# Kernel tuning notes

Hardware: AMD Instinct MI355X
Metric: run time of the kernel (lower is better)

The kernel has to match this reference:

```python
import jax, jax.numpy as jnp
import numpy as np

N = 20000        # number of protein atoms
C_IN = 32        # input atom features
C = 128          # hidden_channels
E_BOND = 80000   # directed bond edges (~2 bonds/atom, both directions)
R = 4.0          # radius_graph radius (Angstrom)
BOX = 55.0       # box side -> ~32 neighbors within r=4


def _radius_graph_np(pos, r):
    # symmetric radius graph, no self loops (PyG radius_graph, neighbor cap omitted)
    r2 = r * r
    rows, cols = [], []
    for i0 in range(0, pos.shape[0], 500):
        chunk = pos[i0:i0 + 500]
        d2 = ((chunk[:, None, :] - pos[None, :, :]) ** 2).sum(-1)
        m = d2 < r2
        m[np.arange(chunk.shape[0]), i0 + np.arange(chunk.shape[0])] = False
        ii, jj = np.nonzero(m)
        rows.append(jj)            # source j
        cols.append(ii + i0)       # target i
    return np.stack([np.concatenate(rows), np.concatenate(cols)]).astype(np.int32)


def setup_inputs() -> dict:
    key = jax.random.key(0)
    ks = jax.random.split(key, 12)
    rng = np.random.default_rng(0)

    pos = rng.uniform(0.0, BOX, (N, 3)).astype(np.float32)
    r_edge_index = jnp.asarray(_radius_graph_np(pos, R))

    half = E_BOND // 2
    s = rng.integers(0, N, half); d = rng.integers(0, N, half)
    edge_index = jnp.asarray(np.stack([np.concatenate([s, d]), np.concatenate([d, s])]).astype(np.int32))

    def lin(k, fin, fout):
        lim = 1.0 / np.sqrt(fin)
        kw, kb = jax.random.split(k)
        W = jax.random.uniform(kw, (fin, fout), jnp.float32, -lim, lim)
        b = jax.random.uniform(kb, (fout,), jnp.float32, -lim, lim)
        return W, b

    We1, be1 = lin(ks[0], C_IN, C)
    We2, be2 = lin(ks[1], C, C)
    Wf1, bf1 = lin(ks[2], 2 * C, C); Ws1, bs1 = lin(ks[3], 2 * C, C)
    Wf2, bf2 = lin(ks[4], 2 * C, C); Ws2, bs2 = lin(ks[5], 2 * C, C)
    Wf3, bf3 = lin(ks[6], 2 * C, C); Ws3, bs3 = lin(ks[7], 2 * C, C)
    Wf4, bf4 = lin(ks[8], 2 * C, C); Ws4, bs4 = lin(ks[9], 2 * C, C)

    x_prot = jax.random.normal(ks[10], (N, C_IN), jnp.float32)
    v_prot = jnp.asarray(pos)

    return dict(x_prot=x_prot, v_prot=v_prot, edge_index=edge_index, r_edge_index=r_edge_index,
                We1=We1, be1=be1, We2=We2, be2=be2,
                Wf1=Wf1, bf1=bf1, Ws1=Ws1, bs1=bs1,
                Wf2=Wf2, bf2=bf2, Ws2=Ws2, bs2=bs2,
                Wf3=Wf3, bf3=bf3, Ws3=Ws3, bs3=bs3,
                Wf4=Wf4, bf4=bf4, Ws4=Ws4, bs4=bs4)


def _cgconv(x, ei, Wf, bf, Ws, bs):
    # PyG CGConv: z = [x_i, x_j]; out = x + mean_j sigmoid(lin_f(z)) * softplus(lin_s(z))
    src, dst = ei[0], ei[1]              # source j -> target i
    z = jnp.concatenate([x[dst], x[src]], axis=1)          # [E, 2C]
    msg = jax.nn.sigmoid(z @ Wf + bf) * jax.nn.softplus(z @ Ws + bs)  # [E, C]
    agg = jax.ops.segment_sum(msg, dst, num_segments=x.shape[0])
    cnt = jax.ops.segment_sum(jnp.ones((ei.shape[1],), x.dtype), dst, num_segments=x.shape[0])
    return x + agg / jnp.maximum(cnt, 1.0)[:, None]


def reference(x_prot, v_prot, edge_index, r_edge_index,
              We1, be1, We2, be2,
              Wf1, bf1, Ws1, bs1, Wf2, bf2, Ws2, bs2,
              Wf3, bf3, Ws3, bs3, Wf4, bf4, Ws4, bs4):
    # embed MLP (PyG MLP with batch-norm at init == identity): Linear->ReLU->Linear
    x = jax.nn.relu(x_prot @ We1 + be1) @ We2 + be2
    # bond convs
    x = jax.nn.relu(_cgconv(x, edge_index, Wf1, bf1, Ws1, bs1))
    x = jax.nn.relu(_cgconv(x, edge_index, Wf2, bf2, Ws2, bs2))
    # radius convs (r_edge_index = radius_graph(v_prot, r=4), precomputed in setup)
    x = jax.nn.relu(_cgconv(x, r_edge_index, Wf3, bf3, Ws3, bs3))
    x = jax.nn.relu(_cgconv(x, r_edge_index, Wf4, bf4, Ws4, bs4))
    return jax.nn.relu(x)  # final self.act (idempotent on ReLU output)
```

## Files before the change

### kernel.cpp

```cpp
#include <hip/hip_runtime.h>
#include <hip/hip_bf16.h>

#define NN 20000
#define CC 128

typedef __attribute__((ext_vector_type(8))) _Float16 half8;
typedef __attribute__((ext_vector_type(2))) _Float16 half2v;
typedef __attribute__((ext_vector_type(4))) float f32x4;

typedef const __attribute__((address_space(1))) void gv_t;
typedef __attribute__((address_space(3))) void sv_t;

__global__ __launch_bounds__(256) void conv_all_kernel(
    const float* __restrict__ Wf0, const float* __restrict__ Ws0,
    const float* __restrict__ Wf1, const float* __restrict__ Ws1,
    const float* __restrict__ Wf2, const float* __restrict__ Ws2,
    const float* __restrict__ Wf3, const float* __restrict__ Ws3,
    const float* __restrict__ We2, const float* __restrict__ We1,
    const float* __restrict__ xprot,
    _Float16* __restrict__ WctAll, _Float16* __restrict__ Wcte,
    _Float16* __restrict__ Wt1, _Float16* __restrict__ xp16) {
    int id = blockIdx.x * 256 + threadIdx.x;
    if (id < 262144) {
        int Lw = id >> 16;
        int i = id & 65535;
        int c = i & 511;
        int k = i >> 9;
        const float* Wfp = (Lw == 0) ? Wf0 : (Lw == 1) ? Wf1 : (Lw == 2) ? Wf2 : Wf3;
        const float* Wsp = (Lw == 0) ? Ws0 : (Lw == 1) ? Ws1 : (Lw == 2) ? Ws2 : Ws3;
        float v;
        if (c < 128) v = Wfp[k * 128 + c];
        else if (c < 256) v = Wfp[(128 + k) * 128 + (c - 128)];
        else if (c < 384) v = Wsp[k * 128 + (c - 256)];
        else v = Wsp[(128 + k) * 128 + (c - 384)];
        WctAll[Lw * 65536 + c * 128 + k] = (_Float16)v;
    } else if (id < 278528) {
        int i = id - 262144;
        int c = i & 127;
        int k = i >> 7;
        Wcte[c * 128 + k] = (_Float16)We2[k * 128 + c];
    } else if (id < 282624) {
        int i = id - 278528;
        int c = i & 127;
        int k = i >> 7;
        Wt1[c * 32 + k] = (_Float16)We1[k * 128 + c];
    } else {
        int i = id - 282624;
        xp16[i] = (_Float16)xprot[i];
    }
}

__global__ __launch_bounds__(256) void enc1_mfma_kernel(
    const _Float16* __restrict__ A, const _Float16* __restrict__ Wt1,
    const float* __restrict__ b, _Float16* __restrict__ Y) {
    int t = threadIdx.x;
    int wid = t >> 6, l = t & 63;
    int lr = l & 15, hi = l >> 4;
    int m0 = blockIdx.x * 128 + wid * 32;
    half8 af[2];
#pragma unroll
    for (int m = 0; m < 2; ++m) {
        int row = m0 + m * 16 + lr;
        half8 v = {0, 0, 0, 0, 0, 0, 0, 0};
        if (row < NN) v = *(const half8*)(A + (long)row * 32 + hi * 8);
        af[m] = v;
    }
    f32x4 acc[2][8] = {};
#pragma unroll
    for (int n = 0; n < 8; ++n) {
        int col = n * 16 + lr;
        half8 bg = *(const half8*)(Wt1 + (long)col * 32 + hi * 8);
#pragma unroll
        for (int m = 0; m < 2; ++m)
            acc[m][n] = __builtin_amdgcn_mfma_f32_16x16x32_f16(af[m], bg, acc[m][n], 0, 0, 0);
    }
#pragma unroll
    for (int n = 0; n < 8; ++n) {
        int col = n * 16 + lr;
        float bb = b[col];
#pragma unroll
        for (int m = 0; m < 2; ++m) {
#pragma unroll
            for (int q = 0; q < 4; ++q) {
                int row = m0 + m * 16 + hi * 4 + q;
                if (row < NN)
                    Y[(long)row * 128 + col] = (_Float16)fmaxf(acc[m][n][q] + bb, 0.0f);
            }
        }
    }
}

__global__ __launch_bounds__(256) void gemm_mfma_kernel(
    const _Float16* __restrict__ A, const _Float16* __restrict__ Wt,
    const float* __restrict__ bias0, const float* __restrict__ bias1,
    char* __restrict__ outH, float* __restrict__ outF,
    _Float16* __restrict__ outF16, int M, int mode) {
    __shared__ _Float16 lds[32768];
    int t = threadIdx.x;
    int w = t >> 6, l = t & 63;
    int m0 = blockIdx.x * 128;
    int n0 = blockIdx.y * 128;
    {
        int rin = l >> 4;
        int cs = l & 15;
#pragma unroll
        for (int j = 0; j < 8; ++j) {
            int r = w * 32 + j * 4 + rin;
            int g = cs ^ (r & 7);
            int grow = m0 + r;
            if (grow > M - 1) grow = M - 1;
            __builtin_amdgcn_global_load_lds((gv_t*)(A + (long)grow * 128 + g * 8),
                (sv_t*)&lds[(w * 32 + j * 4) * 128], 16, 0, 0);
            __builtin_amdgcn_global_load_lds((gv_t*)(Wt + (long)(n0 + r) * 128 + g * 8),
                (sv_t*)&lds[16384 + (w * 32 + j * 4) * 128], 16, 0, 0);
        }
    }
    __syncthreads();
    int wm = w >> 1, wn = w & 1;
    int lr = l & 15, hi = l >> 4;
    f32x4 acc[4][4] = {};
#pragma unroll
    for (int ks = 0; ks < 4; ++ks) {
        int cidx = 4 * ks + hi;
        half8 af[4], bg[4];
#pragma unroll
        for (int m = 0; m < 4; ++m) {
            int row = wm * 64 + m * 16 + lr;
            af[m] = *(const half8*)(&lds[row * 128 + (cidx ^ (row & 7)) * 8]);
        }
#pragma unroll
        for (int n = 0; n < 4; ++n) {
            int row = wn * 64 + n * 16 + lr;
            bg[n] = *(const half8*)(&lds[16384 + row * 128 + (cidx ^ (row & 7)) * 8]);
        }
#pragma unroll
        for (int m = 0; m < 4; ++m)
#pragma unroll
            for (int n = 0; n < 4; ++n)
                acc[m][n] = __builtin_amdgcn_mfma_f32_16x16x32_f16(
                    af[m], bg[n], acc[m][n], 0, 0, 0);
    }
    if (mode == 0) {
        __syncthreads();
        const float S = 1.44269504f;
        bool isSrc = (n0 == 128) || (n0 == 384);
        float sgn = (n0 == 128) ? -S : S;
#pragma unroll
        for (int n = 0; n < 4; ++n) {
            int cl = wn * 64 + n * 16 + lr;
            int gcol = n0 + cl;
            float badd = (gcol < 128) ? bias0[gcol]
                       : ((gcol >= 256 && gcol < 384) ? bias1[gcol - 256] : 0.0f);
#pragma unroll
            for (int m = 0; m < 4; ++m)
#pragma unroll
                for (int q = 0; q < 4; ++q) {
                    int rl = wm * 64 + m * 16 + hi * 4 + q;
                    float v = acc[m][n][q] + badd;
                    if (!isSrc) {
                        lds[rl * 144 + cl] = (_Float16)(v * S);
                    } else {
                        float p = __builtin_amdgcn_exp2f(v * sgn);
                        uint b = __float_as_uint(p);
                        b = (b + 0x7FFFu + ((b >> 16) & 1u)) >> 16;
                        ((ushort*)lds)[rl * 144 + cl] = (ushort)b;
                    }
                }
        }
        __syncthreads();
        int base = (n0 == 0) ? 0 : (n0 == 128) ? 512 : (n0 == 256) ? 256 : 768;
#pragma unroll
        for (int i = 0; i < 8; ++i) {
            int id = t + 256 * i;
            int row = id >> 4, ch = id & 15;
            int grow = m0 + row;
            if (grow < M) {
                half8 v = *(const half8*)(&lds[row * 144 + ch * 8]);
                *(half8*)(outH + (long)grow * 1024 + base + ch * 16) = v;
            }
        }
    } else {
#pragma unroll
        for (int n = 0; n < 4; ++n) {
            int gcol = n0 + wn * 64 + n * 16 + lr;
            float badd = bias0[gcol];
#pragma unroll
            for (int m = 0; m < 4; ++m)
#pragma unroll
                for (int q = 0; q < 4; ++q) {
                    int grow = m0 + wm * 64 + m * 16 + hi * 4 + q;
                    if (grow < M) {
                        float v = acc[m][n][q] + badd;
                        outF[(long)grow * 128 + gcol] = v;
                        outF16[(long)grow * 128 + gcol] = (_Float16)v;
                    }
                }
        }
    }
}

__global__ __launch_bounds__(256) void count_int_kernel(
    const int* __restrict__ dst, int E, int* __restrict__ cnt) {
    int e = blockIdx.x * 256 + threadIdx.x;
    if (e < E) atomicAdd(&cnt[dst[e]], 1);
}

__global__ __launch_bounds__(1024) void scan_kernel(
    const int* __restrict__ cnt, int* __restrict__ off) {
    __shared__ int part[1024];
    int t = threadIdx.x;
    int base = t * 20;
    int loc[20];
    int s = 0;
#pragma unroll
    for (int i = 0; i < 20; ++i) {
        int idx = base + i;
        int v = (idx < NN) ? cnt[idx] : 0;
        loc[i] = s;
        s += v;
    }
    part[t] = s;
    __syncthreads();
    for (int d = 1; d < 1024; d <<= 1) {
        int v = (t >= d) ? part[t - d] : 0;
        __syncthreads();
        part[t] += v;
        __syncthreads();
    }
    int pre = (t > 0) ? part[t - 1] : 0;
#pragma unroll
    for (int i = 0; i < 20; ++i) {
        int idx = base + i;
        if (idx < NN) off[idx] = pre + loc[i];
    }
    if (t == 1023) off[NN] = part[1023];
}

__global__ __launch_bounds__(256) void scatter_kernel(
    const int* __restrict__ src, const int* __restrict__ dst, int E,
    const int* __restrict__ off, int* __restrict__ cur, int* __restrict__ eid) {
    int e = blockIdx.x * 256 + threadIdx.x;
    if (e < E) {
        int d = dst[e];
        int p = off[d] + atomicAdd(&cur[d], 1);
        eid[p] = src[e];
    }
}

__global__ __launch_bounds__(256) void csr_off_kernel(
    const int* __restrict__ dst, int E, int N1, int* __restrict__ off) {
    int n = blockIdx.x * 256 + threadIdx.x;
    if (n >= N1) return;
    int lo = 0, hi = E;
    while (lo < hi) {
        int mid = (lo + hi) >> 1;
        if (dst[mid] < n) lo = mid + 1;
        else hi = mid;
    }
    off[n] = lo;
}

__global__ __launch_bounds__(256) void node_agg_kernel(
    const char* __restrict__ H, const int* __restrict__ srcArr,
    const int* __restrict__ off, const float* __restrict__ xin,
    float* __restrict__ xout, _Float16* __restrict__ xh, int write_h) {
    int n = blockIdx.x * 4 + (threadIdx.x >> 6);
    int nu = __builtin_amdgcn_readfirstlane(n);
    int l = threadIdx.x & 63;
    const char* hb = H + (long)nu * 1024;
    half2v fdh = *(const half2v*)(hb + l * 4);
    half2v sdh = *(const half2v*)(hb + 256 + l * 4);
    float vd0 = __builtin_amdgcn_exp2f(-(float)fdh.x);
    float vd1 = __builtin_amdgcn_exp2f(-(float)fdh.y);
    float ud0 = __builtin_amdgcn_exp2f((float)sdh.x);
    float ud1 = __builtin_amdgcn_exp2f((float)sdh.y);
    int e0 = __builtin_amdgcn_readfirstlane(off[nu]);
    int e1 = __builtin_amdgcn_readfirstlane(off[nu + 1]);
    float ax = 0.0f, ay = 0.0f;
#define EDGEC(w0, w1)                                                        \
    {                                                                        \
        float vs0 = __uint_as_float((w0) << 16);                             \
        float vs1 = __uint_as_float((w0) & 0xFFFF0000u);                     \
        float us0 = __uint_as_float((w1) << 16);                             \
        float us1 = __uint_as_float((w1) & 0xFFFF0000u);                     \
        float rx = __builtin_amdgcn_rcpf(__builtin_fmaf(vd0, vs0, 1.0f));    \
        float ry = __builtin_amdgcn_rcpf(__builtin_fmaf(vd1, vs1, 1.0f));    \
        float px = __builtin_amdgcn_logf(__builtin_fmaf(ud0, us0, 1.0f));    \
        float py = __builtin_amdgcn_logf(__builtin_fmaf(ud1, us1, 1.0f));    \
        ax = __builtin_fmaf(rx, px, ax);                                     \
        ay = __builtin_fmaf(ry, py, ay);                                     \
    }
    int e = e0;
    for (; e + 7 < e1; e += 8) {
        uint wv[8], wu[8];
#pragma unroll
        for (int j = 0; j < 8; ++j) {
            int s = srcArr[e + j];
            const char* hs = H + (long)s * 1024 + (long)l * 4;
            wv[j] = *(const uint*)(hs + 512);
            wu[j] = *(const uint*)(hs + 768);
        }
#pragma unroll
        for (int j = 0; j < 8; ++j) EDGEC(wv[j], wu[j])
    }
    for (; e < e1; ++e) {
        int s = srcArr[e];
        const char* hs = H + (long)s * 1024 + (long)l * 4;
        uint w0 = *(const uint*)(hs + 512);
        uint w1 = *(const uint*)(hs + 768);
        EDGEC(w0, w1)
    }
#undef EDGEC
    float inv = 0.6931471805599453f *
                __builtin_amdgcn_rcpf(fmaxf((float)(e1 - e0), 1.0f));
    float2 xv = ((const float2*)xin)[(long)nu * 64 + l];
    float ox = fmaxf(xv.x + ax * inv, 0.0f);
    float oy = fmaxf(xv.y + ay * inv, 0.0f);
    ((float2*)xout)[(long)nu * 64 + l] = make_float2(ox, oy);
    if (write_h) {
        half2v oh;
        oh.x = (_Float16)ox;
        oh.y = (_Float16)oy;
        ((half2v*)xh)[(long)nu * 64 + l] = oh;
    }
}

extern "C" void kernel_launch(void* const* d_in, const int* in_sizes, int n_in,
                              void* d_out, int out_size, void* d_ws, size_t ws_size,
                              hipStream_t stream) {
    const float* x_prot = (const float*)d_in[0];
    const int* eb = (const int*)d_in[2];
    const int* er = (const int*)d_in[3];
    int Eb = in_sizes[2] / 2;
    int Er = in_sizes[3] / 2;
    const float* We1 = (const float*)d_in[4];
    const float* be1 = (const float*)d_in[5];
    const float* We2 = (const float*)d_in[6];
    const float* be2 = (const float*)d_in[7];
    const float* Wf[4]  = {(const float*)d_in[8],  (const float*)d_in[12],
                           (const float*)d_in[16], (const float*)d_in[20]};
    const float* bf[4]  = {(const float*)d_in[9],  (const float*)d_in[13],
                           (const float*)d_in[17], (const float*)d_in[21]};
    const float* Wsp[4] = {(const float*)d_in[10], (const float*)d_in[14],
                           (const float*)d_in[18], (const float*)d_in[22]};
    const float* bsp[4] = {(const float*)d_in[11], (const float*)d_in[15],
                           (const float*)d_in[19], (const float*)d_in[23]};

    char* ws = (char*)d_ws;
    float*     xbuf  = (float*)ws;
    _Float16*  xhf   = (_Float16*)(ws + 10240000);
    char*      H     = (char*)(ws + 15360000);
    _Float16*  xp16  = (_Float16*)(ws + 35840000);
    int*       cntI  = (int*)(ws + 37120000);
    int*       curB  = (int*)(ws + 37200000);
    int*       offB  = (int*)(ws + 37280000);
    int*       offR  = (int*)(ws + 37360016);
    int*       eidB  = (int*)(ws + 37440032);
    _Float16*  WctAll= (_Float16*)(ws + 37760032);
    _Float16*  Wcte  = (_Float16*)(ws + 38284320);
    _Float16*  Wt1   = (_Float16*)(ws + 38317088);

    const int* srcB = eb;
    const int* dstB = eb + Eb;
    const int* srcR = er;

    conv_all_kernel<<<3604, 256, 0, stream>>>(
        Wf[0], Wsp[0], Wf[1], Wsp[1], Wf[2], Wsp[2], Wf[3], Wsp[3],
        We2, We1, x_prot, WctAll, Wcte, Wt1, xp16);

    hipMemsetAsync(cntI, 0, 160000, stream);
    count_int_kernel<<<(Eb + 255) / 256, 256, 0, stream>>>(dstB, Eb, cntI);
    scan_kernel<<<1, 1024, 0, stream>>>(cntI, offB);
    scatter_kernel<<<(Eb + 255) / 256, 256, 0, stream>>>(srcB, dstB, Eb, offB, curB, eidB);
    csr_off_kernel<<<(NN + 256) / 256, 256, 0, stream>>>(er + Er, Er, NN + 1, offR);

    enc1_mfma_kernel<<<157, 256, 0, stream>>>(xp16, Wt1, be1, (_Float16*)H);
    {
        dim3 g(157, 1);
        gemm_mfma_kernel<<<g, 256, 0, stream>>>((_Float16*)H, Wcte, be2, be2,
                                                nullptr, xbuf, xhf, NN, 1);
    }

    for (int L = 0; L < 4; ++L) {
        dim3 g(157, 4);
        gemm_mfma_kernel<<<g, 256, 0, stream>>>(xhf, WctAll + L * 65536, bf[L],
                                                bsp[L], H, nullptr, nullptr, NN, 0);
        const int* sArr = (L < 2) ? eidB : srcR;
        const int* oArr = (L < 2) ? offB : offR;
        float* xout = (L == 3) ? (float*)d_out : xbuf;
        node_agg_kernel<<<NN / 4, 256, 0, stream>>>(H, sArr, oArr, xbuf, xout,
                                                    xhf, (L == 3) ? 0 : 1);
    }
    (void)n_in; (void)out_size; (void)ws_size;
}
```

Before: 243.1 us.

## Interleave source H halves, drop fp32 residual buffer, double-buffer edge gathers

The GEMM epilogue now interleaves the two source-side halves of H so each lane fetches one 8-byte word per neighbor instead of two 4-byte loads. The fp32 residual copy of x is removed, and node aggregation reads and updates the fp16 x in place, writing fp32 only for the final layer. The edge loop is restructured to prefetch the next batch of 8 neighbors while computing the current one, with a 4-wide remainder path. Together these cut gather transactions and residual traffic but add fp16 rounding of the residual stream between layers. The in-place update relies on the GEMM having consumed x before aggregation runs.

Measured after the change: 269.8 us. 1.11x slower.

```diff
diff --git a/kernel.cpp b/kernel.cpp
--- a/kernel.cpp
+++ b/kernel.cpp
@@ -93,8 +93,7 @@
 __global__ __launch_bounds__(256) void gemm_mfma_kernel(
     const _Float16* __restrict__ A, const _Float16* __restrict__ Wt,
     const float* __restrict__ bias0, const float* __restrict__ bias1,
-    char* __restrict__ outH, float* __restrict__ outF,
-    _Float16* __restrict__ outF16, int M, int mode) {
+    char* __restrict__ outH, _Float16* __restrict__ outF16, int M, int mode) {
     __shared__ _Float16 lds[32768];
     int t = threadIdx.x;
     int w = t >> 6, l = t & 63;
@@ -168,15 +167,23 @@
                 }
         }
         __syncthreads();
-        int base = (n0 == 0) ? 0 : (n0 == 128) ? 512 : (n0 == 256) ? 256 : 768;
+        bool isSrc2 = (n0 == 128) || (n0 == 384);
 #pragma unroll
         for (int i = 0; i < 8; ++i) {
             int id = t + 256 * i;
             int row = id >> 4, ch = id & 15;
             int grow = m0 + row;
-            if (grow < M) {
-                half8 v = *(const half8*)(&lds[row * 144 + ch * 8]);
-                *(half8*)(outH + (long)grow * 1024 + base + ch * 16) = v;
+            if (grow >= M) continue;
+            half8 v = *(const half8*)(&lds[row * 144 + ch * 8]);
+            if (!isSrc2) {
+                int b2 = (n0 == 0) ? 0 : 256;
+                *(half8*)(outH + (long)grow * 1024 + b2 + ch * 16) = v;
+            } else {
+                const uint* vp = (const uint*)&v;
+                char* bp = outH + (long)grow * 1024 + 512 + ch * 32 +
+                           ((n0 == 384) ? 4 : 0);
+#pragma unroll
+                for (int j = 0; j < 4; ++j) *(uint*)(bp + j * 8) = vp[j];
             }
         }
     } else {
@@ -189,11 +196,9 @@
 #pragma unroll
                 for (int q = 0; q < 4; ++q) {
                     int grow = m0 + wm * 64 + m * 16 + hi * 4 + q;
-                    if (grow < M) {
-                        float v = acc[m][n][q] + badd;
-                        outF[(long)grow * 128 + gcol] = v;
-                        outF16[(long)grow * 128 + gcol] = (_Float16)v;
-                    }
+                    if (grow < M)
+                        outF16[(long)grow * 128 + gcol] =
+                            (_Float16)(acc[m][n][q] + badd);
                 }
         }
     }
@@ -262,12 +267,13 @@
 
 __global__ __launch_bounds__(256) void node_agg_kernel(
     const char* __restrict__ H, const int* __restrict__ srcArr,
-    const int* __restrict__ off, const float* __restrict__ xin,
-    float* __restrict__ xout, _Float16* __restrict__ xh, int write_h) {
+    const int* __restrict__ off, _Float16* __restrict__ xh,
+    float* __restrict__ xoutF, int write_h) {
     int n = blockIdx.x * 4 + (threadIdx.x >> 6);
     int nu = __builtin_amdgcn_readfirstlane(n);
     int l = threadIdx.x & 63;
     const char* hb = H + (long)nu * 1024;
+    half2v xv = ((const half2v*)xh)[(long)nu * 64 + l];
     half2v fdh = *(const half2v*)(hb + l * 4);
     half2v sdh = *(const half2v*)(hb + 256 + l * 4);
     float vd0 = __builtin_amdgcn_exp2f(-(float)fdh.x);
@@ -290,38 +296,71 @@
         ax = __builtin_fmaf(rx, px, ax);                                     \
         ay = __builtin_fmaf(ry, py, ay);                                     \
     }
+    int B = (e1 - e0) >> 3;
     int e = e0;
-    for (; e + 7 < e1; e += 8) {
-        uint wv[8], wu[8];
+    if (B > 0) {
+        uint2 wa[8], wb[8];
 #pragma unroll
         for (int j = 0; j < 8; ++j) {
             int s = srcArr[e + j];
-            const char* hs = H + (long)s * 1024 + (long)l * 4;
-            wv[j] = *(const uint*)(hs + 512);
-            wu[j] = *(const uint*)(hs + 768);
-        }
-#pragma unroll
-        for (int j = 0; j < 8; ++j) EDGEC(wv[j], wu[j])
+            wa[j] = *(const uint2*)(H + (long)s * 1024 + 512 + (long)l * 8);
+        }
+        for (int i = 0; i + 1 < B; ++i) {
+            int eb = e + 8 * (i + 1);
+            if (i & 1) {
+#pragma unroll
+                for (int j = 0; j < 8; ++j) {
+                    int s = srcArr[eb + j];
+                    wa[j] = *(const uint2*)(H + (long)s * 1024 + 512 + (long)l * 8);
+                }
+#pragma unroll
+                for (int j = 0; j < 8; ++j) EDGEC(wb[j].x, wb[j].y)
+            } else {
+#pragma unroll
+                for (int j = 0; j < 8; ++j) {
+                    int s = srcArr[eb + j];
+                    wb[j] = *(const uint2*)(H + (long)s * 1024 + 512 + (long)l * 8);
+                }
+#pragma unroll
+                for (int j = 0; j < 8; ++j) EDGEC(wa[j].x, wa[j].y)
+            }
+        }
+        if ((B - 1) & 1) {
+#pragma unroll
+            for (int j = 0; j < 8; ++j) EDGEC(wb[j].x, wb[j].y)
+        } else {
+#pragma unroll
+            for (int j = 0; j < 8; ++j) EDGEC(wa[j].x, wa[j].y)
+        }
+        e += 8 * B;
+    }
+    for (; e + 3 < e1; e += 4) {
+        uint2 w0, w1, w2, w3;
+        int s0 = srcArr[e], s1 = srcArr[e + 1];
+        int s2 = srcArr[e + 2], s3 = srcArr[e + 3];
+        w0 = *(const uint2*)(H + (long)s0 * 1024 + 512 + (long)l * 8);
+        w1 = *(const uint2*)(H + (long)s1 * 1024 + 512 + (long)l * 8);
+        w2 = *(const uint2*)(H + (long)s2 * 1024 + 512 + (long)l * 8);
+        w3 = *(const uint2*)(H + (long)s3 * 1024 + 512 + (long)l * 8);
+        EDGEC(w0.x, w0.y) EDGEC(w1.x, w1.y) EDGEC(w2.x, w2.y) EDGEC(w3.x, w3.y)
     }
     for (; e < e1; ++e) {
         int s = srcArr[e];
-        const char* hs = H + (long)s * 1024 + (long)l * 4;
-        uint w0 = *(const uint*)(hs + 512);
-        uint w1 = *(const uint*)(hs + 768);
-        EDGEC(w0, w1)
+        uint2 w0 = *(const uint2*)(H + (long)s * 1024 + 512 + (long)l * 8);
+        EDGEC(w0.x, w0.y)
     }
 #undef EDGEC
     float inv = 0.6931471805599453f *
                 __builtin_amdgcn_rcpf(fmaxf((float)(e1 - e0), 1.0f));
-    float2 xv = ((const float2*)xin)[(long)nu * 64 + l];
-    float ox = fmaxf(xv.x + ax * inv, 0.0f);
-    float oy = fmaxf(xv.y + ay * inv, 0.0f);
-    ((float2*)xout)[(long)nu * 64 + l] = make_float2(ox, oy);
+    float ox = fmaxf((float)xv.x + ax * inv, 0.0f);
+    float oy = fmaxf((float)xv.y + ay * inv, 0.0f);
     if (write_h) {
         half2v oh;
         oh.x = (_Float16)ox;
         oh.y = (_Float16)oy;
         ((half2v*)xh)[(long)nu * 64 + l] = oh;
+    } else {
+        ((float2*)xoutF)[(long)nu * 64 + l] = make_float2(ox, oy);
     }
 }
 
@@ -347,18 +386,17 @@
                            (const float*)d_in[19], (const float*)d_in[23]};
 
     char* ws = (char*)d_ws;
-    float*     xbuf  = (float*)ws;
-    _Float16*  xhf   = (_Float16*)(ws + 10240000);
-    char*      H     = (char*)(ws + 15360000);
-    _Float16*  xp16  = (_Float16*)(ws + 35840000);
-    int*       cntI  = (int*)(ws + 37120000);
-    int*       curB  = (int*)(ws + 37200000);
-    int*       offB  = (int*)(ws + 37280000);
-    int*       offR  = (int*)(ws + 37360016);
-    int*       eidB  = (int*)(ws + 37440032);
-    _Float16*  WctAll= (_Float16*)(ws + 37760032);
-    _Float16*  Wcte  = (_Float16*)(ws + 38284320);
-    _Float16*  Wt1   = (_Float16*)(ws + 38317088);
+    _Float16*  xhf   = (_Float16*)ws;
+    char*      H     = (char*)(ws + 5120000);
+    _Float16*  xp16  = (_Float16*)(ws + 25600000);
+    int*       cntI  = (int*)(ws + 26880000);
+    int*       curB  = (int*)(ws + 26960000);
+    int*       offB  = (int*)(ws + 27040000);
+    int*       offR  = (int*)(ws + 27120016);
+    int*       eidB  = (int*)(ws + 27200032);
+    _Float16*  WctAll= (_Float16*)(ws + 27520032);
+    _Float16*  Wcte  = (_Float16*)(ws + 28044320);
+    _Float16*  Wt1   = (_Float16*)(ws + 28077088);
 
     const int* srcB = eb;
     const int* dstB = eb + Eb;
@@ -378,18 +416,18 @@
     {
         dim3 g(157, 1);
         gemm_mfma_kernel<<<g, 256, 0, stream>>>((_Float16*)H, Wcte, be2, be2,
-                                                nullptr, xbuf, xhf, NN, 1);
+                                                nullptr, xhf, NN, 1);
     }
 
     for (int L = 0; L < 4; ++L) {
         dim3 g(157, 4);
         gemm_mfma_kernel<<<g, 256, 0, stream>>>(xhf, WctAll + L * 65536, bf[L],
-                                                bsp[L], H, nullptr, nullptr, NN, 0);
+                                                bsp[L], H, nullptr, NN, 0);
         const int* sArr = (L < 2) ? eidB : srcR;
         const int* oArr = (L < 2) ? offB : offR;
-        float* xout = (L == 3) ? (float*)d_out : xbuf;
-        node_agg_kernel<<<NN / 4, 256, 0, stream>>>(H, sArr, oArr, xbuf, xout,
-                                                    xhf, (L == 3) ? 0 : 1);
+        node_agg_kernel<<<NN / 4, 256, 0, stream>>>(H, sArr, oArr, xhf,
+                                                    (float*)d_out,
+                                                    (L == 3) ? 0 : 1);
     }
     (void)n_in; (void)out_size; (void)ws_size;
 }
```
